# Performance work log

Hardware: AMD Instinct MI355X
Metric: run time of the kernel (lower is better)

The kernel has to match this reference:

```python
import jax, jax.numpy as jnp
import numpy as np

B, K, D, V = 4096, 128, 512, 128000


def setup_inputs() -> dict:
    key = jax.random.key(0)
    k1, k2, k3 = jax.random.split(key, 3)
    inp = jax.random.normal(k1, (B, D), dtype=jnp.float32)
    indices = jax.random.randint(k2, (B, K), 0, V, dtype=jnp.int64)
    # xavier_uniform: bound = sqrt(6/(fan_in+fan_out)) for weight [V, D]
    bound = float(np.sqrt(6.0 / (V + D)))
    weight = jax.random.uniform(k3, (V, D), dtype=jnp.float32, minval=-bound, maxval=bound)
    bias = jnp.zeros((V,), dtype=jnp.float32)
    return {"inp": inp, "indices": indices, "sparse": 1, "weight": weight, "bias": bias}


def reference(inp, indices, sparse, weight, bias):
    if sparse:
        # gather per-sample weight rows [B, K, D] and bias [B, K], then batched dot
        w = weight[indices]          # [B, K, D]
        b = bias[indices]            # [B, K]
        out = jnp.einsum('bkd,bd->bk', w, inp) + b
        return out
    else:
        return inp @ weight.T + bias
```

## Files before the change

kernel.cpp:

```cpp
#include <hip/hip_runtime.h>


constexpr int Kc = 128;
constexpr int Dc = 512;

__global__ __launch_bounds__(256) void SparseProjection_kernel(
    const float* __restrict__ inp,
    const int*   __restrict__ indices,
    const float* __restrict__ weight,
    const float* __restrict__ bias,
    float*       __restrict__ out)
{
    const int b    = blockIdx.x;
    const int tid  = threadIdx.x;
    const int lane = tid & 63;
    const int wave = tid >> 6;

    const float4* inp_row = (const float4*)(inp + (size_t)b * Dc);
    const float4 a0 = inp_row[lane];
    const float4 a1 = inp_row[64 + lane];

    const int* idx_base  = indices + (size_t)b * Kc;
    float*     out_base  = out     + (size_t)b * Kc;

    #pragma unroll 4
    for (int i = 0; i < 32; ++i) {
        const int k   = wave * 32 + i;
        const int idx = idx_base[k];
        const float4* wrow = (const float4*)(weight + (size_t)idx * Dc);

        const float4 w0 = wrow[lane];
        const float4 w1 = wrow[64 + lane];

        float s = a0.x * w0.x + a0.y * w0.y + a0.z * w0.z + a0.w * w0.w
                + a1.x * w1.x + a1.y * w1.y + a1.z * w1.z + a1.w * w1.w;

        #pragma unroll
        for (int off = 32; off > 0; off >>= 1)
            s += __shfl_xor(s, off, 64);

        if (lane == 0)
            out_base[k] = s + bias[idx];
    }
}

extern "C" void kernel_launch(void* const* d_in, const int* in_sizes, int n_in,
                              void* d_out, int out_size, void* d_ws, size_t ws_size,
                              hipStream_t stream) {
    const float* inp     = (const float*)d_in[0];
    const int*   indices = (const int*)  d_in[1];
    const float* weight  = (const float*)d_in[3];
    const float* bias    = (const float*)d_in[4];
    float*       out     = (float*)d_out;

    const int B = in_sizes[0] / Dc;
    SparseProjection_kernel<<<B, 256, 0, stream>>>(inp, indices, weight, bias, out);
}
```

Baseline: 448.4 us.

## Bucket samples by vocab row so each weight row is read once

Replaces the per-sample gather of weight rows with a counting-sort inversion. A histogram, an allocation pass and a scatter pass build, for every vocab row, the list of (sample, k) pairs that use it. A compute kernel then loads each needed weight row once and loops over its users, gathering the small input rows instead. The goal is to cut the roughly 1 GB of random weight-row traffic down to about one pass over the weight matrix. The cost is three extra kernel launches, a memset, global atomics, scattered output writes and a workspace requirement, with a fallback to the original kernel when the workspace is too small.

After: 493.1 us. 1.1x slower.

```diff
diff --git a/kernel.cpp b/kernel.cpp
--- a/kernel.cpp
+++ b/kernel.cpp
@@ -1,36 +1,79 @@
 #include <hip/hip_runtime.h>
 
 
+constexpr int Bc = 4096;
 constexpr int Kc = 128;
 constexpr int Dc = 512;
+constexpr int Vc = 128000;
+constexpr int NB = Bc * Kc;
 
-__global__ __launch_bounds__(256) void SparseProjection_kernel(
+constexpr size_t WS_HIST   = 0;
+constexpr size_t WS_CURSOR = 512000;
+constexpr size_t WS_START  = 512256;
+constexpr size_t WS_CUR    = 1024256;
+constexpr size_t WS_PAIRS  = 1536256;
+constexpr size_t WS_NEED   = WS_PAIRS + (size_t)NB * 4;
+
+__global__ __launch_bounds__(256) void hist_kernel(
+    const int* __restrict__ indices, unsigned* __restrict__ hist)
+{
+    int i = blockIdx.x * 256 + threadIdx.x;
+    if (i < NB) atomicAdd(&hist[indices[i]], 1u);
+}
+
+__global__ __launch_bounds__(256) void alloc_kernel(
+    const unsigned* __restrict__ hist, unsigned* __restrict__ start,
+    unsigned* __restrict__ cur, unsigned* __restrict__ cursor)
+{
+    int v = blockIdx.x * 256 + threadIdx.x;
+    if (v < Vc) {
+        unsigned c = hist[v];
+        unsigned s = c ? atomicAdd(cursor, c) : 0u;
+        start[v] = s;
+        cur[v]   = s;
+    }
+}
+
+__global__ __launch_bounds__(256) void scatter_kernel(
+    const int* __restrict__ indices, unsigned* __restrict__ cur,
+    unsigned* __restrict__ pairs)
+{
+    int i = blockIdx.x * 256 + threadIdx.x;
+    if (i < NB) {
+        int v = indices[i];
+        unsigned pos = atomicAdd(&cur[v], 1u);
+        pairs[pos] = (unsigned)i;
+    }
+}
+
+__global__ __launch_bounds__(256) void compute_kernel(
     const float* __restrict__ inp,
-    const int*   __restrict__ indices,
     const float* __restrict__ weight,
     const float* __restrict__ bias,
-    float*       __restrict__ out)
+    const unsigned* __restrict__ hist,
+    const unsigned* __restrict__ start,
+    const unsigned* __restrict__ pairs,
+    float* __restrict__ out)
 {
-    const int b    = blockIdx.x;
-    const int tid  = threadIdx.x;
-    const int lane = tid & 63;
-    const int wave = tid >> 6;
+    const int wave = threadIdx.x >> 6;
+    const int lane = threadIdx.x & 63;
+    const int v    = blockIdx.x * 4 + wave;
 
-    const float4* inp_row = (const float4*)(inp + (size_t)b * Dc);
-    const float4 a0 = inp_row[lane];
-    const float4 a1 = inp_row[64 + lane];
+    const unsigned cnt = hist[v];
+    if (cnt == 0) return;
+    const unsigned st = start[v];
 
-    const int* idx_base  = indices + (size_t)b * Kc;
-    float*     out_base  = out     + (size_t)b * Kc;
+    const float4* wrow = (const float4*)(weight + (size_t)v * Dc);
+    const float4 w0 = wrow[lane];
+    const float4 w1 = wrow[64 + lane];
+    const float  bv = bias[v];
 
-    #pragma unroll 4
-    for (int i = 0; i < 32; ++i) {
-        const int k   = wave * 32 + i;
-        const int idx = idx_base[k];
-        const float4* wrow = (const float4*)(weight + (size_t)idx * Dc);
-
-        const float4 w0 = wrow[lane];
-        const float4 w1 = wrow[64 + lane];
+    for (unsigned e = 0; e < cnt; ++e) {
+        const unsigned i = pairs[st + e];
+        const unsigned b = i >> 7;
+        const float4* arow = (const float4*)(inp + (size_t)b * Dc);
+        const float4 a0 = arow[lane];
+        const float4 a1 = arow[64 + lane];
 
         float s = a0.x * w0.x + a0.y * w0.y + a0.z * w0.z + a0.w * w0.w
                 + a1.x * w1.x + a1.y * w1.y + a1.z * w1.z + a1.w * w1.w;
@@ -39,8 +82,33 @@
         for (int off = 32; off > 0; off >>= 1)
             s += __shfl_xor(s, off, 64);
 
-        if (lane == 0)
-            out_base[k] = s + bias[idx];
+        if (lane == 0) out[i] = s + bv;
+    }
+}
+
+__global__ __launch_bounds__(256) void fallback_kernel(
+    const float* __restrict__ inp, const int* __restrict__ indices,
+    const float* __restrict__ weight, const float* __restrict__ bias,
+    float* __restrict__ out)
+{
+    const int b = blockIdx.x, lane = threadIdx.x & 63, wave = threadIdx.x >> 6;
+    const float4* inp_row = (const float4*)(inp + (size_t)b * Dc);
+    const float4 a0 = inp_row[lane];
+    const float4 a1 = inp_row[64 + lane];
+    const int* idx_base = indices + (size_t)b * Kc;
+    float* out_base = out + (size_t)b * Kc;
+    #pragma unroll 4
+    for (int i = 0; i < 32; ++i) {
+        const int k = wave * 32 + i;
+        const int idx = idx_base[k];
+        const float4* wrow = (const float4*)(weight + (size_t)idx * Dc);
+        const float4 w0 = wrow[lane];
+        const float4 w1 = wrow[64 + lane];
+        float s = a0.x * w0.x + a0.y * w0.y + a0.z * w0.z + a0.w * w0.w
+                + a1.x * w1.x + a1.y * w1.y + a1.z * w1.z + a1.w * w1.w;
+        #pragma unroll
+        for (int off = 32; off > 0; off >>= 1) s += __shfl_xor(s, off, 64);
+        if (lane == 0) out_base[k] = s + bias[idx];
     }
 }
 
@@ -53,6 +121,23 @@
     const float* bias    = (const float*)d_in[4];
     float*       out     = (float*)d_out;
 
-    const int B = in_sizes[0] / Dc;
-    SparseProjection_kernel<<<B, 256, 0, stream>>>(inp, indices, weight, bias, out);
+    if (ws_size < WS_NEED) {
+        fallback_kernel<<<Bc, 256, 0, stream>>>(inp, indices, weight, bias, out);
+        return;
+    }
+
+    char* ws = (char*)d_ws;
+    unsigned* hist   = (unsigned*)(ws + WS_HIST);
+    unsigned* cursor = (unsigned*)(ws + WS_CURSOR);
+    unsigned* start  = (unsigned*)(ws + WS_START);
+    unsigned* cur    = (unsigned*)(ws + WS_CUR);
+    unsigned* pairs  = (unsigned*)(ws + WS_PAIRS);
+
+    hipMemsetAsync(ws, 0, WS_START, stream);
+
+    hist_kernel   <<<(NB + 255) / 256, 256, 0, stream>>>(indices, hist);
+    alloc_kernel  <<<(Vc + 255) / 256, 256, 0, stream>>>(hist, start, cur, cursor);
+    scatter_kernel<<<(NB + 255) / 256, 256, 0, stream>>>(indices, cur, pairs);
+    compute_kernel<<<Vc / 4,            256, 0, stream>>>(inp, weight, bias,
+                                                          hist, start, pairs, out);
 }
```
